# Kernel tuning notes

Measured on AMD Instinct MI355X. Metric: run time of the kernel, lower is better.

## Reference

```python
import jax, jax.numpy as jnp
import numpy as np
import math

EMBED_DIM = 1024
NUM_HEADS = 16
NUM_KV_HEADS = 16
DEPTH = 12
HEAD_DIM = EMBED_DIM // NUM_HEADS // 2  # 32
LAMBDA_INIT = 0.8 - 0.6 * math.exp(-0.3 * DEPTH)
EPS = 1e-5
THETA = 0.0001


def rope(q):
    # q: (b, s, h, d) with interleaved pairs, matches apply_rotary_pos_emb
    b, s, h, d = q.shape
    pos = jnp.arange(s, dtype=jnp.float32)[:, None]                      # (s,1)
    freq = 1.0 / (THETA ** (2.0 * jnp.arange(d // 2, dtype=jnp.float32) / d))
    ang = pos * freq                                                     # (s, d/2)
    cos = jnp.cos(ang)[None, :, None, :].astype(q.dtype)
    sin = jnp.sin(ang)[None, :, None, :].astype(q.dtype)
    qr = q.reshape(b, s, h, d // 2, 2)
    q0, q1 = qr[..., 0], qr[..., 1]
    out = jnp.stack([q0 * cos - q1 * sin, q0 * sin + q1 * cos], axis=-1)
    return out.reshape(q.shape)


def setup_inputs() -> dict:
    key = jax.random.key(0)
    ks = jax.random.split(key, 10)
    d = EMBED_DIM
    sd = 1.0 / math.sqrt(d)
    return {
        "x": jax.random.normal(ks[0], (1, 2048, d), dtype=jnp.float32),
        "Wq": jax.random.normal(ks[1], (d, d), dtype=jnp.float32) * sd,
        "Wk": jax.random.normal(ks[2], (d, d), dtype=jnp.float32) * sd,
        "Wv": jax.random.normal(ks[3], (d, d), dtype=jnp.float32) * sd,
        "Wo": jax.random.normal(ks[4], (d, d), dtype=jnp.float32) * sd,
        "lambda_q1": jax.random.normal(ks[5], (HEAD_DIM,), dtype=jnp.float32) * 0.1,
        "lambda_k1": jax.random.normal(ks[6], (HEAD_DIM,), dtype=jnp.float32) * 0.1,
        "lambda_q2": jax.random.normal(ks[7], (HEAD_DIM,), dtype=jnp.float32) * 0.1,
        "lambda_k2": jax.random.normal(ks[8], (HEAD_DIM,), dtype=jnp.float32) * 0.1,
        "subln_g": jnp.ones((2 * HEAD_DIM,), dtype=jnp.float32),
    }


def reference(x, Wq, Wk, Wv, Wo, lambda_q1, lambda_k1, lambda_q2, lambda_k2, subln_g):
    b, s, d = x.shape
    H, hd = NUM_HEADS, HEAD_DIM
    scaling = hd ** (-0.5)

    q = (x @ Wq).reshape(b, s, 2 * H, hd)
    k = (x @ Wk).reshape(b, s, 2 * NUM_KV_HEADS, hd)
    v = (x @ Wv).reshape(b, s, NUM_KV_HEADS, 2 * hd)

    q = rope(q).transpose(0, 2, 1, 3) * scaling   # (b, 2H, s, hd)
    k = rope(k).transpose(0, 2, 1, 3)             # (b, 2H, s, hd)  (n_rep = 1)
    v = v.transpose(0, 2, 1, 3)                   # (b, H, s, 2hd)

    scores = jnp.einsum("bhqd,bhkd->bhqk", q, k)  # (b, 2H, s, s)
    probs = jax.nn.softmax(scores.astype(jnp.float32), axis=-1).astype(scores.dtype)

    lam1 = jnp.exp(jnp.sum(lambda_q1 * lambda_k1))
    lam2 = jnp.exp(jnp.sum(lambda_q2 * lambda_k2))
    lam = (lam1 - lam2 + LAMBDA_INIT).astype(q.dtype)

    probs = probs.reshape(b, H, 2, s, s)
    w = probs[:, :, 0] - lam * probs[:, :, 1]     # (b, H, s, s)

    attn = jnp.einsum("bhqk,bhkd->bhqd", w, v)    # (b, H, s, 2hd)
    rms = jax.lax.rsqrt(jnp.mean(attn * attn, axis=-1, keepdims=True) + EPS)
    attn = attn * rms * subln_g
    attn = attn * (1.0 - LAMBDA_INIT)

    attn = attn.transpose(0, 2, 1, 3).reshape(b, s, H * 2 * hd)
    return attn @ Wo
```

## Files before the change

kernel.cpp:

```cpp
#include <hip/hip_runtime.h>
#include <math.h>

#define S 2048
#define D 1024
#define NH 16
#define HD 32
#define HD2 64

static constexpr float SCALE_Q_EXP2  = 0.17677669529663687f * 1.4426950408889634f;
static constexpr float LAMBDA_INIT_F = 0.78360576653162450f;
static constexpr float ONE_MINUS_LI  = 0.21639423346837553f;

typedef unsigned short u16;
typedef unsigned int   u32;
typedef __attribute__((ext_vector_type(4)))  unsigned short u16x4;
typedef __attribute__((ext_vector_type(8)))  short          bfrag;
typedef __attribute__((ext_vector_type(16))) float          f16acc;
typedef __attribute__((ext_vector_type(4)))  unsigned int   uint4v;

__device__ __forceinline__ u16 f2bf(float f) {
    u32 u = __builtin_bit_cast(u32, f);
    return (u16)((u + 0x7FFFu + ((u >> 16) & 1u)) >> 16);
}
__device__ __forceinline__ f16acc fillv(float v) {
    f16acc z;
#pragma unroll
    for (int i = 0; i < 16; ++i) z[i] = v;
    return z;
}
__device__ __forceinline__ float exp2_raw(float x) {
#if __has_builtin(__builtin_amdgcn_exp2f)
    return __builtin_amdgcn_exp2f(x);
#else
    float r;
    asm volatile("v_exp_f32 %0, %1\n\ts_nop 1" : "=v"(r) : "v"(x));
    return r;
#endif
}
#define MFMA(a, b, c) __builtin_amdgcn_mfma_f32_32x32x16_bf16(a, b, c, 0, 0, 0)

__device__ __forceinline__ void gload16(const u16* src, u16* lds) {
    __builtin_amdgcn_global_load_lds((const __attribute__((address_space(1))) void*)src,
                                     (__attribute__((address_space(3))) void*)lds, 16, 0, 0);
}

__global__ void prep_kernel(const float* __restrict__ lq1, const float* __restrict__ lk1,
                            const float* __restrict__ lq2, const float* __restrict__ lk2,
                            float* __restrict__ cosT, float* __restrict__ sinT,
                            float* __restrict__ lamOut) {
    int idx = blockIdx.x * blockDim.x + threadIdx.x;
    if (idx < S * 16) {
        int p = idx >> 4;
        int m = idx & 15;
        const double base = (double)1.0e-4f;
        float pf   = (float)pow(base, (double)m * (1.0 / 16.0));
        float freq = 1.0f / pf;
        float angf = (float)p * freq;
        double a = (double)angf;
        cosT[idx] = (float)cos(a);
        sinT[idx] = (float)sin(a);
    }
    if (blockIdx.x == 0 && threadIdx.x == 0) {
        float s1 = 0.f, s2 = 0.f;
        for (int i = 0; i < HD; ++i) {
            s1 += lq1[i] * lk1[i];
            s2 += lq2[i] * lk2[i];
        }
        *lamOut = expf(s1) - expf(s2) + LAMBDA_INIT_F;
    }
}

__global__ __launch_bounds__(256)
void convert_kernel(const float* __restrict__ x,  const float* __restrict__ Wq,
                    const float* __restrict__ Wk, const float* __restrict__ Wv,
                    const float* __restrict__ Wo,
                    u16* __restrict__ xb,  u16* __restrict__ WqT, u16* __restrict__ WkT,
                    u16* __restrict__ WvT, u16* __restrict__ WoT) {
    const int z = blockIdx.y;
    if (z == 0) {
        const int i = blockIdx.x * 256 + threadIdx.x;
        const float4 v = *(const float4*)&x[(size_t)i * 4];
        u16x4 r; r.x = f2bf(v.x); r.y = f2bf(v.y); r.z = f2bf(v.z); r.w = f2bf(v.w);
        *(u16x4*)&xb[(size_t)i * 4] = r;
        return;
    }
    const int b = blockIdx.x;
    if (b >= 256) return;
    __shared__ u16 Ts[64][66];
    const float* W = (z == 1) ? Wq : (z == 2) ? Wk : (z == 3) ? Wv : Wo;
    u16* T = (z == 1) ? WqT : (z == 2) ? WkT : (z == 3) ? WvT : WoT;
    const int k0 = (b >> 4) * 64, n0 = (b & 15) * 64;
    const int rg = threadIdx.x >> 4, cc = (threadIdx.x & 15) * 4;
#pragma unroll
    for (int i = 0; i < 4; ++i) {
        const int r = rg * 4 + i;
        const float4 v = *(const float4*)&W[(size_t)(k0 + r) * D + n0 + cc];
        Ts[r][cc + 0] = f2bf(v.x); Ts[r][cc + 1] = f2bf(v.y);
        Ts[r][cc + 2] = f2bf(v.z); Ts[r][cc + 3] = f2bf(v.w);
    }
    __syncthreads();
#pragma unroll
    for (int i = 0; i < 4; ++i) {
        const int rn = rg * 4 + i;
        u16x4 res;
        res.x = Ts[cc + 0][rn]; res.y = Ts[cc + 1][rn];
        res.z = Ts[cc + 2][rn]; res.w = Ts[cc + 3][rn];
        *(u16x4*)&T[(size_t)(n0 + rn) * D + k0 + cc] = res;
    }
}

template<int MODE>
__global__ __launch_bounds__(256)
void mm_kernel(const u16* __restrict__ Ab, const u16* __restrict__ B0,
               const u16* __restrict__ B1, const u16* __restrict__ B2,
               const float* __restrict__ cosT, const float* __restrict__ sinT,
               u16* __restrict__ Qb, u16* __restrict__ Kb2, u16* __restrict__ VT,
               float* __restrict__ Of) {
    __shared__ u16 As[128 * 32];
    __shared__ u16 Bs[128 * 32];

    const int nb   = blockIdx.x;
    const int row0 = blockIdx.y * 128;
    const int tid  = threadIdx.x;
    const int wave = tid >> 6;
    const int lane = tid & 63;
    const int ql   = lane & 31;
    const int hi   = lane >> 5;
    const int wr   = wave >> 1;
    const int wc   = wave & 1;

    const u16* Bt;
    int col0B;
    if (MODE == 0) {
        Bt = (nb < 8) ? B0 : (nb < 16) ? B1 : B2;
        col0B = (nb & 7) * 128;
    } else {
        Bt = B0;
        col0B = nb * 128;
    }

    const int rIn  = lane >> 2;
    const int kof  = 8 * (lane & 3);
    const size_t aRow0 = (size_t)(row0 + 16 * wave       + rIn) * D + kof;
    const size_t aRow1 = (size_t)(row0 + 16 * (wave + 4) + rIn) * D + kof;
    const size_t bRow0 = (size_t)(col0B + 16 * wave       + rIn) * D + kof;
    const size_t bRow1 = (size_t)(col0B + 16 * (wave + 4) + rIn) * D + kof;
    u16* ldsA0 = &As[512 * wave + 8 * lane];
    u16* ldsA1 = &As[512 * (wave + 4) + 8 * lane];
    u16* ldsB0 = &Bs[512 * wave + 8 * lane];
    u16* ldsB1 = &Bs[512 * (wave + 4) + 8 * lane];

    const int aoff = (wr * 64 + ql) * 32 + hi * 8;
    const int boff = (wc * 64 + ql) * 32 + hi * 8;

    f16acc acc00 = fillv(0.f), acc01 = fillv(0.f), acc10 = fillv(0.f), acc11 = fillv(0.f);

    for (int kk = 0; kk < D; kk += 32) {
        gload16(Ab + aRow0 + kk, ldsA0);
        gload16(Ab + aRow1 + kk, ldsA1);
        gload16(Bt + bRow0 + kk, ldsB0);
        gload16(Bt + bRow1 + kk, ldsB1);
        __syncthreads();
#pragma unroll
        for (int ks = 0; ks < 2; ++ks) {
            const bfrag a0 = *(const bfrag*)&As[aoff + ks * 16];
            const bfrag a1 = *(const bfrag*)&As[aoff + 32 * 32 + ks * 16];
            const bfrag b0 = *(const bfrag*)&Bs[boff + ks * 16];
            const bfrag b1 = *(const bfrag*)&Bs[boff + 32 * 32 + ks * 16];
            acc00 = MFMA(a0, b0, acc00);
            acc01 = MFMA(a0, b1, acc01);
            acc10 = MFMA(a1, b0, acc10);
            acc11 = MFMA(a1, b1, acc11);
        }
        __syncthreads();
    }

    f16acc accA[2][2];
    accA[0][0] = acc00; accA[0][1] = acc01; accA[1][0] = acc10; accA[1][1] = acc11;

    if (MODE == 0 && nb < 8) {
        const int m = ql >> 1;
        const bool ev = (ql & 1) == 0;
#pragma unroll
        for (int i = 0; i < 2; ++i)
#pragma unroll
        for (int j = 0; j < 2; ++j) {
            const int n = (nb & 7) * 128 + wc * 64 + j * 32 + ql;
            const int head = n >> 5;
            u16* hb = Qb + (size_t)head * S * HD;
#pragma unroll
            for (int r = 0; r < 16; ++r) {
                const int row = row0 + wr * 64 + i * 32 + 4 * hi + (r & 3) + 8 * (r >> 2);
                const float self = accA[i][j][r];
                const float part = __shfl_xor(self, 1);
                const float c = cosT[(row << 4) + m], s = sinT[(row << 4) + m];
                const float res = ev ? (self * c - part * s) : (part * s + self * c);
                hb[(size_t)row * HD + ql] = f2bf(res * SCALE_Q_EXP2);
            }
        }
    } else if (MODE == 0 && nb < 16) {
        const int m = ql >> 1;
        const bool ev = (ql & 1) == 0;
#pragma unroll
        for (int i = 0; i < 2; ++i)
#pragma unroll
        for (int j = 0; j < 2; ++j) {
            const int n = (nb & 7) * 128 + wc * 64 + j * 32 + ql;
            const int h2 = n >> 5;
            u16* hb = Kb2 + (size_t)h2 * 65536;
#pragma unroll
            for (int r = 0; r < 16; ++r) {
                const int row = row0 + wr * 64 + i * 32 + 4 * hi + (r & 3) + 8 * (r >> 2);
                const float self = accA[i][j][r];
                const float part = __shfl_xor(self, 1);
                const float c = cosT[(row << 4) + m], s = sinT[(row << 4) + m];
                const float res = ev ? (self * c - part * s) : (part * s + self * c);
                const int idx = (row >> 5) * 1024 + (row & 31) * 32
                              + (((ql >> 3) ^ (row & 3)) << 3) + (ql & 7);
                hb[idx] = f2bf(res);
            }
        }
    } else if (MODE == 0) {
#pragma unroll
        for (int i = 0; i < 2; ++i)
#pragma unroll
        for (int j = 0; j < 2; ++j) {
            const int n = (nb & 7) * 128 + wc * 64 + j * 32 + ql;
            const int head = n >> 6, d = n & 63;
            u16* tb = VT + (size_t)head * 131072;
#pragma unroll
            for (int q = 0; q < 4; ++q) {
                const int row = row0 + wr * 64 + i * 32 + 4 * hi + 8 * q;
                const int off = (d * 32 + (row & 31)) ^ ((d & 3) << 3);
                u16x4 res;
                res.x = f2bf(accA[i][j][4 * q + 0]);
                res.y = f2bf(accA[i][j][4 * q + 1]);
                res.z = f2bf(accA[i][j][4 * q + 2]);
                res.w = f2bf(accA[i][j][4 * q + 3]);
                *(u16x4*)&tb[(size_t)(row >> 5) * 2048 + off] = res;
            }
        }
    } else {
#pragma unroll
        for (int i = 0; i < 2; ++i)
#pragma unroll
        for (int j = 0; j < 2; ++j) {
            const int gcol = col0B + wc * 64 + j * 32 + ql;
#pragma unroll
            for (int r = 0; r < 16; ++r) {
                const int row = row0 + wr * 64 + i * 32 + 4 * hi + (r & 3) + 8 * (r >> 2);
                Of[(size_t)row * D + gcol] = accA[i][j][r];
            }
        }
    }
}

__global__ __launch_bounds__(512, 2)
void attn_mfma(const u16* __restrict__ Qb, const u16* __restrict__ Kb2,
               const u16* __restrict__ Vt2, const float* __restrict__ lamPtr,
               const float* __restrict__ g, u16* __restrict__ AO) {
    const int h    = blockIdx.y;
    const int tid  = threadIdx.x;
    const int wave = tid >> 6;
    const int lane = tid & 63;
    const int hi   = lane >> 5;
    const int ql   = lane & 31;
    const int t    = wave >> 2;
    const int wv   = wave & 3;
    const int q0   = (blockIdx.x * 2 + t) * 32;
    const int cbase = wv * 16;

    __shared__ __align__(16) u16 KV[2][4][4096];
    float (*CMB)[64][66] = (float(*)[64][66])&KV[0][0][0];

    const u16* qp1 = Qb + ((size_t)(2 * h) * S + q0 + ql) * HD + 8 * hi;
    const u16* qp2 = qp1 + (size_t)S * HD;
    bfrag qf1[2], qf2[2];
    qf1[0] = *(const bfrag*)(qp1);      qf1[1] = *(const bfrag*)(qp1 + 16);
    qf2[0] = *(const bfrag*)(qp2);      qf2[1] = *(const bfrag*)(qp2 + 16);

    const u16* k1g = Kb2 + (size_t)(2 * h) * 65536;
    const u16* k2g = k1g + 65536;
    const u16* vg  = Vt2 + (size_t)h * 131072;

    int pofs[2];
#pragma unroll
    for (int s = 0; s < 2; ++s) pofs[s] = (((2 * s + hi) ^ (ql & 3)) << 3);

    const f16acc ZR = fillv(0.f);
    uint4v ou; ou[0] = ou[1] = ou[2] = ou[3] = 0x3F803F80u;
    const bfrag ONES = __builtin_bit_cast(bfrag, ou);

    f16acc acc1[2], acc2[2];
    acc1[0] = fillv(0.f); acc1[1] = fillv(0.f);
    acc2[0] = fillv(0.f); acc2[1] = fillv(0.f);
    float l1 = 0.f, l2 = 0.f;

    auto stage = [&](int buf, int c) {
        u16* base = &KV[buf][wv][0];
        if (t == 0) {
            const u16* k1 = k1g + (size_t)c * 1024;
            const u16* k2 = k2g + (size_t)c * 1024;
            gload16(k1 + lane * 8,       base + lane * 8);
            gload16(k1 + 512 + lane * 8, base + 512 + lane * 8);
            gload16(k2 + lane * 8,       base + 1024 + lane * 8);
            gload16(k2 + 512 + lane * 8, base + 1536 + lane * 8);
        } else {
            const u16* vv = vg + (size_t)c * 2048;
            gload16(vv + lane * 8,        base + 2048 + lane * 8);
            gload16(vv + 512 + lane * 8,  base + 2560 + lane * 8);
            gload16(vv + 1024 + lane * 8, base + 3072 + lane * 8);
            gload16(vv + 1536 + lane * 8, base + 3584 + lane * 8);
        }
    };

    stage(0, cbase);
    __syncthreads();
    int cur = 0;

    for (int i = 0; i < 16; ++i) {
        if (i < 15) stage(cur ^ 1, cbase + i + 1);

        const u16* Kq = &KV[cur][wv][0];
        bfrag kc1[2], kc2[2], vc[2][2];
#pragma unroll
        for (int s = 0; s < 2; ++s) {
            kc1[s] = *(const bfrag*)(Kq + ql * 32 + pofs[s]);
            kc2[s] = *(const bfrag*)(Kq + 1024 + ql * 32 + pofs[s]);
#pragma unroll
            for (int dt = 0; dt < 2; ++dt)
                vc[s][dt] = *(const bfrag*)(Kq + 2048 + (dt * 32 + ql) * 32 + pofs[s]);
        }

        __builtin_amdgcn_s_setprio(1);
        f16acc s1 = MFMA(kc1[0], qf1[0], ZR);  s1 = MFMA(kc1[1], qf1[1], s1);
        f16acc s2 = MFMA(kc2[0], qf2[0], ZR);  s2 = MFMA(kc2[1], qf2[1], s2);
        __builtin_amdgcn_s_setprio(0);

#pragma unroll
        for (int r = 0; r < 16; ++r) {
            s1[r] = exp2_raw(s1[r]);
            s2[r] = exp2_raw(s2[r]);
        }

        u32 w1[8], w2[8];
#pragma unroll
        for (int j = 0; j < 8; ++j) {
            asm("v_cvt_pk_bf16_f32 %0, %1, %2" : "=v"(w1[j]) : "v"(s1[2 * j]), "v"(s1[2 * j + 1]));
            asm("v_cvt_pk_bf16_f32 %0, %1, %2" : "=v"(w2[j]) : "v"(s2[2 * j]), "v"(s2[2 * j + 1]));
        }
        asm("v_permlane32_swap_b32 %0, %1" : "+v"(w1[0]), "+v"(w1[2]));
        asm("v_permlane32_swap_b32 %0, %1" : "+v"(w1[1]), "+v"(w1[3]));
        asm("v_permlane32_swap_b32 %0, %1" : "+v"(w1[4]), "+v"(w1[6]));
        asm("v_permlane32_swap_b32 %0, %1" : "+v"(w1[5]), "+v"(w1[7]));
        asm("v_permlane32_swap_b32 %0, %1" : "+v"(w2[0]), "+v"(w2[2]));
        asm("v_permlane32_swap_b32 %0, %1" : "+v"(w2[1]), "+v"(w2[3]));
        asm("v_permlane32_swap_b32 %0, %1" : "+v"(w2[4]), "+v"(w2[6]));
        asm("v_permlane32_swap_b32 %0, %1" : "+v"(w2[5]), "+v"(w2[7]));
        uint4v u;
        bfrag p1[2], p2[2];
        u[0] = w1[0]; u[1] = w1[1]; u[2] = w1[2]; u[3] = w1[3];
        p1[0] = __builtin_bit_cast(bfrag, u);
        u[0] = w1[4]; u[1] = w1[5]; u[2] = w1[6]; u[3] = w1[7];
        p1[1] = __builtin_bit_cast(bfrag, u);
        u[0] = w2[0]; u[1] = w2[1]; u[2] = w2[2]; u[3] = w2[3];
        p2[0] = __builtin_bit_cast(bfrag, u);
        u[0] = w2[4]; u[1] = w2[5]; u[2] = w2[6]; u[3] = w2[7];
        p2[1] = __builtin_bit_cast(bfrag, u);

        __builtin_amdgcn_s_setprio(1);
        acc1[0] = MFMA(vc[0][0], p1[0], acc1[0]);
        acc1[0] = MFMA(vc[1][0], p1[1], acc1[0]);
        acc1[1] = MFMA(vc[0][1], p1[0], acc1[1]);
        acc1[1] = MFMA(vc[1][1], p1[1], acc1[1]);
        acc2[0] = MFMA(vc[0][0], p2[0], acc2[0]);
        acc2[0] = MFMA(vc[1][0], p2[1], acc2[0]);
        acc2[1] = MFMA(vc[0][1], p2[0], acc2[1]);
        acc2[1] = MFMA(vc[1][1], p2[1], acc2[1]);
        f16acc t1 = MFMA(ONES, p1[0], ZR);  t1 = MFMA(ONES, p1[1], t1);
        f16acc t2 = MFMA(ONES, p2[0], ZR);  t2 = MFMA(ONES, p2[1], t2);
        __builtin_amdgcn_s_setprio(0);
        l1 += t1[0];
        l2 += t2[0];

        __syncthreads();
        cur ^= 1;
    }

#pragma unroll 1
    for (int p = 1; p < 4; ++p) {
        if (wv == p) {
            float* c0 = &CMB[t][lane][0];
#pragma unroll
            for (int dt = 0; dt < 2; ++dt)
#pragma unroll
                for (int r = 0; r < 16; ++r) {
                    c0[dt * 16 + r]      = acc1[dt][r];
                    c0[32 + dt * 16 + r] = acc2[dt][r];
                }
            c0[64] = l1; c0[65] = l2;
        }
        __syncthreads();
        if (wv == 0) {
            const float* c0 = &CMB[t][lane][0];
#pragma unroll
            for (int dt = 0; dt < 2; ++dt)
#pragma unroll
                for (int r = 0; r < 16; ++r) {
                    acc1[dt][r] += c0[dt * 16 + r];
                    acc2[dt][r] += c0[32 + dt * 16 + r];
                }
            l1 += c0[64]; l2 += c0[65];
        }
        __syncthreads();
    }

    if (wv == 0) {
        const float lam = *lamPtr;
        const float inv1 = 1.0f / l1, inv2 = 1.0f / l2;
        float o_[2][16];
        float ss = 0.f;
#pragma unroll
        for (int dt = 0; dt < 2; ++dt)
#pragma unroll
            for (int r = 0; r < 16; ++r) {
                float o = acc1[dt][r] * inv1 - lam * (acc2[dt][r] * inv2);
                o_[dt][r] = o;
                ss += o * o;
            }
        ss += __shfl_xor(ss, 32);
        const float rs = rsqrtf(ss * (1.0f / 64.0f) + 1e-5f);

        u16* aorow = AO + (size_t)(q0 + ql) * D + h * 64;
#pragma unroll
        for (int dt = 0; dt < 2; ++dt)
#pragma unroll
            for (int G = 0; G < 4; ++G) {
                const int dbase = dt * 32 + G * 8 + hi * 4;
                const float4 gv = *(const float4*)&g[dbase];
                u16x4 res;
                res.x = f2bf(o_[dt][4 * G + 0] * rs * gv.x * ONE_MINUS_LI);
                res.y = f2bf(o_[dt][4 * G + 1] * rs * gv.y * ONE_MINUS_LI);
                res.z = f2bf(o_[dt][4 * G + 2] * rs * gv.z * ONE_MINUS_LI);
                res.w = f2bf(o_[dt][4 * G + 3] * rs * gv.w * ONE_MINUS_LI);
                *(u16x4*)&aorow[dbase] = res;
            }
    }
}

extern "C" void kernel_launch(void* const* d_in, const int* in_sizes, int n_in,
                              void* d_out, int out_size, void* d_ws, size_t ws_size,
                              hipStream_t stream) {
    const float* x   = (const float*)d_in[0];
    const float* Wq  = (const float*)d_in[1];
    const float* Wk  = (const float*)d_in[2];
    const float* Wv  = (const float*)d_in[3];
    const float* Wo  = (const float*)d_in[4];
    const float* lq1 = (const float*)d_in[5];
    const float* lk1 = (const float*)d_in[6];
    const float* lq2 = (const float*)d_in[7];
    const float* lk2 = (const float*)d_in[8];
    const float* g   = (const float*)d_in[9];
    float* out = (float*)d_out;

    char* ws = (char*)d_ws;
    float* cosT = (float*)(ws);
    float* sinT = (float*)(ws + 131072);
    float* lam  = (float*)(ws + 262144);
    char*  b    = ws + 262400;
    u16*   Qb   = (u16*)(b);
    u16*   Kb2  = (u16*)(b + 4194304);
    u16*   VT   = (u16*)(b + 8388608);
    u16*   AO   = (u16*)(b + 12582912);
    u16*   xb   = (u16*)(b + 16777216);
    u16*   WqT  = (u16*)(b + 20971520);
    u16*   WkT  = (u16*)(b + 23068672);
    u16*   WvT  = (u16*)(b + 25165824);
    u16*   WoT  = (u16*)(b + 27262976);

    prep_kernel<<<128, 256, 0, stream>>>(lq1, lk1, lq2, lk2, cosT, sinT, lam);
    convert_kernel<<<dim3(2048, 5), 256, 0, stream>>>(x, Wq, Wk, Wv, Wo,
                                                      xb, WqT, WkT, WvT, WoT);

    mm_kernel<0><<<dim3(24, 16), 256, 0, stream>>>(xb, WqT, WkT, WvT, cosT, sinT,
                                                   Qb, Kb2, VT, nullptr);

    attn_mfma<<<dim3(32, NH), 512, 0, stream>>>(Qb, Kb2, VT, lam, g, AO);

    mm_kernel<1><<<dim3(8, 16), 256, 0, stream>>>(AO, WoT, nullptr, nullptr, cosT, sinT,
                                                  nullptr, nullptr, nullptr, out);
}
```

Measured before the change: 117.1 us.

## Load K/V fragments directly from global into registers and remap attention grid

The K and V producer layouts are rewritten so each lane's MFMA fragment is a contiguous 16-byte chunk. The attention kernel then drops its LDS double-buffer staging and per-iteration __syncthreads, software-pipelining register loads of the next chunk's K/V fragments instead. The attention grid is flattened to 1D, with the block index remapped so consecutive blocks spread across heads, which may improve L2 locality or XCD distribution. This removes LDS traffic and barriers, at the cost of more registers and of relying on global/L2 latency being hidden by the register ping-pong.

```diff
diff --git a/kernel.cpp b/kernel.cpp
--- a/kernel.cpp
+++ b/kernel.cpp
@@ -207,6 +207,8 @@
         for (int j = 0; j < 2; ++j) {
             const int n = (nb & 7) * 128 + wc * 64 + j * 32 + ql;
             const int h2 = n >> 5;
+            const int d  = n & 31;
+            const int dpl = (d >> 3) * 256 + (d & 7);
             u16* hb = Kb2 + (size_t)h2 * 65536;
 #pragma unroll
             for (int r = 0; r < 16; ++r) {
@@ -215,9 +217,7 @@
                 const float part = __shfl_xor(self, 1);
                 const float c = cosT[(row << 4) + m], s = sinT[(row << 4) + m];
                 const float res = ev ? (self * c - part * s) : (part * s + self * c);
-                const int idx = (row >> 5) * 1024 + (row & 31) * 32
-                              + (((ql >> 3) ^ (row & 3)) << 3) + (ql & 7);
-                hb[idx] = f2bf(res);
+                hb[(row >> 5) * 1024 + dpl + (row & 31) * 8] = f2bf(res);
             }
         }
     } else if (MODE == 0) {
@@ -227,17 +227,18 @@
         for (int j = 0; j < 2; ++j) {
             const int n = (nb & 7) * 128 + wc * 64 + j * 32 + ql;
             const int head = n >> 6, d = n & 63;
+            const int dt = d >> 5, dl = d & 31;
             u16* tb = VT + (size_t)head * 131072;
 #pragma unroll
             for (int q = 0; q < 4; ++q) {
                 const int row = row0 + wr * 64 + i * 32 + 4 * hi + 8 * q;
-                const int off = (d * 32 + (row & 31)) ^ ((d & 3) << 3);
+                const int idx = (row >> 5) * 2048 + (dt * 4 + q) * 256 + dl * 8 + 4 * hi;
                 u16x4 res;
                 res.x = f2bf(accA[i][j][4 * q + 0]);
                 res.y = f2bf(accA[i][j][4 * q + 1]);
                 res.z = f2bf(accA[i][j][4 * q + 2]);
                 res.w = f2bf(accA[i][j][4 * q + 3]);
-                *(u16x4*)&tb[(size_t)(row >> 5) * 2048 + off] = res;
+                *(u16x4*)&tb[idx] = res;
             }
         }
     } else {
@@ -259,7 +260,9 @@
 void attn_mfma(const u16* __restrict__ Qb, const u16* __restrict__ Kb2,
                const u16* __restrict__ Vt2, const float* __restrict__ lamPtr,
                const float* __restrict__ g, u16* __restrict__ AO) {
-    const int h    = blockIdx.y;
+    const int bid  = blockIdx.x;
+    const int h    = (bid & 7) * 2 + ((bid >> 3) >> 5);
+    const int bx   = (bid >> 3) & 31;
     const int tid  = threadIdx.x;
     const int wave = tid >> 6;
     const int lane = tid & 63;
@@ -267,11 +270,10 @@
     const int ql   = lane & 31;
     const int t    = wave >> 2;
     const int wv   = wave & 3;
-    const int q0   = (blockIdx.x * 2 + t) * 32;
+    const int q0   = (bx * 2 + t) * 32;
     const int cbase = wv * 16;
 
-    __shared__ __align__(16) u16 KV[2][4][4096];
-    float (*CMB)[64][66] = (float(*)[64][66])&KV[0][0][0];
+    __shared__ float CMB[2][64][66];
 
     const u16* qp1 = Qb + ((size_t)(2 * h) * S + q0 + ql) * HD + 8 * hi;
     const u16* qp2 = qp1 + (size_t)S * HD;
@@ -282,10 +284,7 @@
     const u16* k1g = Kb2 + (size_t)(2 * h) * 65536;
     const u16* k2g = k1g + 65536;
     const u16* vg  = Vt2 + (size_t)h * 131072;
-
-    int pofs[2];
-#pragma unroll
-    for (int s = 0; s < 2; ++s) pofs[s] = (((2 * s + hi) ^ (ql & 3)) << 3);
+    const int kro  = ql * 8;
 
     const f16acc ZR = fillv(0.f);
     uint4v ou; ou[0] = ou[1] = ou[2] = ou[3] = 0x3F803F80u;
@@ -296,40 +295,29 @@
     acc2[0] = fillv(0.f); acc2[1] = fillv(0.f);
     float l1 = 0.f, l2 = 0.f;
 
-    auto stage = [&](int buf, int c) {
-        u16* base = &KV[buf][wv][0];
-        if (t == 0) {
-            const u16* k1 = k1g + (size_t)c * 1024;
-            const u16* k2 = k2g + (size_t)c * 1024;
-            gload16(k1 + lane * 8,       base + lane * 8);
-            gload16(k1 + 512 + lane * 8, base + 512 + lane * 8);
-            gload16(k2 + lane * 8,       base + 1024 + lane * 8);
-            gload16(k2 + 512 + lane * 8, base + 1536 + lane * 8);
-        } else {
-            const u16* vv = vg + (size_t)c * 2048;
-            gload16(vv + lane * 8,        base + 2048 + lane * 8);
-            gload16(vv + 512 + lane * 8,  base + 2560 + lane * 8);
-            gload16(vv + 1024 + lane * 8, base + 3072 + lane * 8);
-            gload16(vv + 1536 + lane * 8, base + 3584 + lane * 8);
-        }
-    };
-
-    stage(0, cbase);
-    __syncthreads();
-    int cur = 0;
-
-    for (int i = 0; i < 16; ++i) {
-        if (i < 15) stage(cur ^ 1, cbase + i + 1);
-
-        const u16* Kq = &KV[cur][wv][0];
-        bfrag kc1[2], kc2[2], vc[2][2];
+    bfrag kA1[2], kA2[2], kB1[2], kB2[2];
+    bfrag vA[2][2], vB[2][2];
+#pragma unroll
+    for (int s = 0; s < 2; ++s) {
+        kA1[s] = *(const bfrag*)(k1g + (size_t)cbase * 1024 + (2 * s + hi) * 256 + kro);
+        kA2[s] = *(const bfrag*)(k2g + (size_t)cbase * 1024 + (2 * s + hi) * 256 + kro);
+#pragma unroll
+        for (int dt = 0; dt < 2; ++dt)
+            vA[s][dt] = *(const bfrag*)(vg + (size_t)cbase * 2048 + (dt * 4 + 2 * s + hi) * 256 + kro);
+    }
+
+    auto body = [&](bfrag (&kc1)[2], bfrag (&kc2)[2], bfrag (&vc)[2][2],
+                    bfrag (&kn1)[2], bfrag (&kn2)[2], bfrag (&vn)[2][2], int cn) {
+        const u16* k1c = k1g + (size_t)cn * 1024;
+        const u16* k2c = k2g + (size_t)cn * 1024;
+        const u16* vvc = vg + (size_t)cn * 2048;
 #pragma unroll
         for (int s = 0; s < 2; ++s) {
-            kc1[s] = *(const bfrag*)(Kq + ql * 32 + pofs[s]);
-            kc2[s] = *(const bfrag*)(Kq + 1024 + ql * 32 + pofs[s]);
+            kn1[s] = *(const bfrag*)(k1c + (2 * s + hi) * 256 + kro);
+            kn2[s] = *(const bfrag*)(k2c + (2 * s + hi) * 256 + kro);
 #pragma unroll
             for (int dt = 0; dt < 2; ++dt)
-                vc[s][dt] = *(const bfrag*)(Kq + 2048 + (dt * 32 + ql) * 32 + pofs[s]);
+                vn[s][dt] = *(const bfrag*)(vvc + (dt * 4 + 2 * s + hi) * 256 + kro);
         }
 
         __builtin_amdgcn_s_setprio(1);
@@ -382,9 +370,13 @@
         __builtin_amdgcn_s_setprio(0);
         l1 += t1[0];
         l2 += t2[0];
-
-        __syncthreads();
-        cur ^= 1;
+    };
+
+    for (int i = 0; i < 16; i += 2) {
+        const int c0 = cbase + i;
+        body(kA1, kA2, vA, kB1, kB2, vB, c0 + 1);
+        const int c2 = (i + 2 < 16) ? c0 + 2 : c0 + 1;
+        body(kB1, kB2, vB, kA1, kA2, vA, c2);
     }
 
 #pragma unroll 1
@@ -485,7 +477,7 @@
     mm_kernel<0><<<dim3(24, 16), 256, 0, stream>>>(xb, WqT, WkT, WvT, cosT, sinT,
                                                    Qb, Kb2, VT, nullptr);
 
-    attn_mfma<<<dim3(32, NH), 512, 0, stream>>>(Qb, Kb2, VT, lam, g, AO);
+    attn_mfma<<<512, 512, 0, stream>>>(Qb, Kb2, VT, lam, g, AO);
 
     mm_kernel<1><<<dim3(8, 16), 256, 0, stream>>>(AO, WoT, nullptr, nullptr, cosT, sinT,
                                                   nullptr, nullptr, nullptr, out);
```

Result: faster. 107.7 us (-8.0%).
